# Kernel tuning notes

Hardware: AMD Instinct MI355X
Metric: run time of the kernel (lower is better)

## Reference

```python
import jax, jax.numpy as jnp
import numpy as np

NUM_HEADS = 16
HEAD_DIM = 64
WINDOW = 512
D_MODEL = NUM_HEADS * HEAD_DIM
BATCH = 2
SEQ = 2048


def setup_inputs() -> dict:
    key = jax.random.key(0)
    k1, k2, k3 = jax.random.split(key, 3)
    x = jax.random.normal(k1, (BATCH, SEQ, D_MODEL), dtype=jnp.float32)
    # Dense layer params (lecun_normal-like scale for stability)
    qkv_kernel = jax.random.normal(k2, (D_MODEL, 3 * NUM_HEADS * HEAD_DIM), dtype=jnp.float32) / np.sqrt(D_MODEL)
    qkv_bias = jnp.zeros((3 * NUM_HEADS * HEAD_DIM,), dtype=jnp.float32)
    out_kernel = jax.random.normal(k3, (NUM_HEADS * HEAD_DIM, D_MODEL), dtype=jnp.float32) / np.sqrt(D_MODEL)
    out_bias = jnp.zeros((D_MODEL,), dtype=jnp.float32)
    return {"x": x, "qkv_kernel": qkv_kernel, "qkv_bias": qkv_bias,
            "out_kernel": out_kernel, "out_bias": out_bias}


def reference(x, qkv_kernel, qkv_bias, out_kernel, out_bias):
    b, s, d = x.shape
    qkv = x @ qkv_kernel + qkv_bias                       # (b, s, 3*H*hd)
    qkv = qkv.reshape(b, s, 3, NUM_HEADS, HEAD_DIM)
    q = qkv[:, :, 0].transpose(0, 2, 1, 3)                # (b, H, s, hd)
    k = qkv[:, :, 1].transpose(0, 2, 1, 3)
    v = qkv[:, :, 2].transpose(0, 2, 1, 3)
    scale = 1.0 / jnp.sqrt(jnp.float32(HEAD_DIM)).astype(x.dtype)
    scores = jnp.einsum('bhqd,bhkd->bhqk', q, k) * scale  # (b, H, s, s)
    rows = jnp.arange(s)[:, None]
    cols = jnp.arange(s)[None, :]
    window_mask = (rows - cols >= 0) & (rows - cols < WINDOW)
    scores = jnp.where(window_mask[None, None], scores, jnp.asarray(-1e9, scores.dtype))
    attn = jax.nn.softmax(scores, axis=-1)
    out = jnp.einsum('bhqk,bhkd->bhqd', attn, v)          # (b, H, s, hd)
    out = out.transpose(0, 2, 1, 3).reshape(b, s, -1)
    return out @ out_kernel + out_bias
```

## Files before the change

### kernel.cpp

```cpp
#include <hip/hip_runtime.h>
#include <cstdint>
#include <cstddef>

#define NUM_HEADS 16
#define HEAD_DIM  64
#define WINDOW    512
#define D_MODEL   1024
#define BATCH     2
#define SEQ       2048
#define MTOT      (BATCH*SEQ)
#define NQKV      (3*D_MODEL)

typedef short bf16x8 __attribute__((ext_vector_type(8)));
typedef float f32x4  __attribute__((ext_vector_type(4)));

__device__ __forceinline__ f32x4 mfma16(bf16x8 a, bf16x8 b, f32x4 c) {
  return __builtin_amdgcn_mfma_f32_16x16x32_bf16(a, b, c, 0, 0, 0);
}

__device__ __forceinline__ unsigned short f2bf(float f) {
  unsigned int u = __float_as_uint(f);
  u += 0x7fffu + ((u >> 16) & 1u);
  return (unsigned short)(u >> 16);
}
__device__ __forceinline__ float bf2f(unsigned short b) {
  return __uint_as_float(((unsigned int)b) << 16);
}

__device__ __forceinline__ void gld16(const unsigned short* g, unsigned short* l) {
  __builtin_amdgcn_global_load_lds(
      (const __attribute__((address_space(1))) unsigned int*)g,
      (__attribute__((address_space(3))) unsigned int*)l, 16, 0, 0);
}

__global__ __launch_bounds__(256) void prep_kernel(const float* __restrict__ x,
                                                   const float* __restrict__ qkv_w,
                                                   const float* __restrict__ out_w,
                                                   unsigned short* __restrict__ Xb,
                                                   unsigned short* __restrict__ Wq,
                                                   unsigned short* __restrict__ Wo) {
  __shared__ float tile[32][33];
  const int bid = blockIdx.x, t = threadIdx.x;
  if (bid < 4096) {
    int i = (bid * 256 + t) * 4;
    float4 v = *(const float4*)(x + i);
    ushort4 o;
    o.x = f2bf(v.x); o.y = f2bf(v.y); o.z = f2bf(v.z); o.w = f2bf(v.w);
    *(ushort4*)(Xb + i) = o;
    return;
  }
  const float* in; unsigned short* out; int R, C, bx, by;
  if (bid < 7168) { int b2 = bid - 4096; in = qkv_w; out = Wq; R = D_MODEL; C = NQKV; bx = b2 % 96; by = b2 / 96; }
  else            { int b2 = bid - 7168; in = out_w; out = Wo; R = D_MODEL; C = D_MODEL; bx = b2 & 31; by = b2 >> 5; }
  int tx = t & 31, ty = t >> 5;
  int c0 = bx * 32, r0 = by * 32;
#pragma unroll
  for (int i = 0; i < 32; i += 8)
    tile[ty + i][tx] = in[(size_t)(r0 + ty + i) * C + c0 + tx];
  __syncthreads();
#pragma unroll
  for (int i = 0; i < 32; i += 8)
    out[(size_t)(c0 + ty + i) * R + r0 + tx] = f2bf(tile[tx][ty + i]);
}

template<bool SWAP, int K>
__device__ __forceinline__ void gemm_mainloop512(const unsigned short* __restrict__ A,
                                                 const unsigned short* __restrict__ Bt,
                                                 int m0, int n0,
                                                 unsigned short* sA, unsigned short* sB,
                                                 f32x4 (&acc)[2][4]) {
  const int t = threadIdx.x;
  const int lane = t & 63, wave = t >> 6;
  const int wr = wave >> 1, wc = wave & 1;
  const int lhi = lane >> 4, llo = lane & 15;
  f32x4 zero = {0.f, 0.f, 0.f, 0.f};
#pragma unroll
  for (int i = 0; i < 2; ++i)
#pragma unroll
    for (int j = 0; j < 4; ++j) acc[i][j] = zero;

  const int cswz = (((t & 3) ^ ((t >> 3) & 3)) << 3);
  const unsigned short* gA = A  + (size_t)(m0 + (t >> 2)) * K + cswz;
  const unsigned short* gB = Bt + (size_t)(n0 + (t >> 2)) * K + cswz;
  const int ldsT = t * 8;
  const int rsw  = (lhi ^ ((llo >> 1) & 3)) * 8;
  const int aoff = (wr * 32 + llo) * 32 + rsw;
  const int boff = (wc * 64 + llo) * 32 + rsw;
  constexpr int nIter = K / 32;

  auto stage = [&](int s) {
    unsigned short* dA = sA + (s % 3) * 4096;
    unsigned short* dB = sB + (s % 3) * 4096;
    gld16(gA + s * 32, dA + ldsT);
    gld16(gB + s * 32, dB + ldsT);
  };

  stage(0);
  stage(1);
#pragma unroll
  for (int it = 0; it < nIter; ++it) {
    if (it + 1 < nIter) asm volatile("s_waitcnt vmcnt(2)\n\ts_barrier" ::: "memory");
    else                asm volatile("s_waitcnt vmcnt(0)\n\ts_barrier" ::: "memory");
    if (it + 2 < nIter) stage(it + 2);
    const unsigned short* cA = sA + (it % 3) * 4096;
    const unsigned short* cB = sB + (it % 3) * 4096;
    bf16x8 af[2], bfr[4];
#pragma unroll
    for (int i = 0; i < 2; ++i) af[i]  = *(const bf16x8*)(cA + aoff + i * 512);
#pragma unroll
    for (int j = 0; j < 4; ++j)  bfr[j] = *(const bf16x8*)(cB + boff + j * 512);
#pragma unroll
    for (int i = 0; i < 2; ++i)
#pragma unroll
      for (int j = 0; j < 4; ++j)
        acc[i][j] = SWAP ? mfma16(bfr[j], af[i], acc[i][j])
                         : mfma16(af[i], bfr[j], acc[i][j]);
  }
}

template<bool SWAP>
__device__ __forceinline__ void gemm_mainloop_256q(const unsigned short* __restrict__ A,
                                                   const unsigned short* __restrict__ Bt,
                                                   int m0, int n0,
                                                   unsigned short* sA, unsigned short* sB,
                                                   f32x4 (&acc)[8][4]) {
  constexpr int K = D_MODEL;
  constexpr int nT = K / 64;
  const int t = threadIdx.x, lane = t & 63, wave = t >> 6;
  const int wr = wave >> 2, wc = wave & 3;
  const int lhi = lane >> 4, llo = lane & 15;
  f32x4 zero = {0.f, 0.f, 0.f, 0.f};
#pragma unroll
  for (int i = 0; i < 8; ++i)
#pragma unroll
    for (int j = 0; j < 4; ++j) acc[i][j] = zero;

  const int r6 = t >> 3;
  const int chunkS = (t & 7) ^ (r6 & 7);
  const unsigned short* gAr = A  + (size_t)(m0 + r6) * K + chunkS * 8;
  const unsigned short* gBr = Bt + (size_t)(n0 + (r6 >> 5) * 64 + (r6 & 31)) * K + chunkS * 8;
  const int dstT = t * 8;

  const int k0off = (lhi ^ (llo & 7)) * 8;
  const int k1off = k0off ^ 32;
  const int aRow = (wr * 64 + llo) * 64;
  const int bRow = (wc * 32 + llo) * 64;

  auto stA = [&](int j, int mh) {
    unsigned short* d = sA + (((j & 1) << 1) + mh) * 8192 + dstT;
    const unsigned short* g = gAr + (size_t)(mh * 64) * K + j * 64;
    gld16(g, d);
    gld16(g + (size_t)128 * K, d + 4096);
  };
  auto stB = [&](int j, int nh) {
    unsigned short* d = sB + (((j & 1) << 1) + nh) * 8192 + dstT;
    const unsigned short* g = gBr + (size_t)(nh * 32) * K + j * 64;
    gld16(g, d);
    gld16(g + (size_t)128 * K, d + 4096);
  };

#define QPHASE(JV, MH, NH, STG)                                                  \
  {                                                                              \
    const unsigned short* cA = sA + ((((JV) & 1) << 1) + (MH)) * 8192;           \
    const unsigned short* cB = sB + ((((JV) & 1) << 1) + (NH)) * 8192;           \
    bf16x8 af[4][2], bfv[2][2];                                                  \
    _Pragma("unroll") for (int i2 = 0; i2 < 4; ++i2) {                           \
      af[i2][0] = *(const bf16x8*)(cA + aRow + i2 * 1024 + k0off);               \
      af[i2][1] = *(const bf16x8*)(cA + aRow + i2 * 1024 + k1off);               \
    }                                                                            \
    _Pragma("unroll") for (int j2 = 0; j2 < 2; ++j2) {                           \
      bfv[j2][0] = *(const bf16x8*)(cB + bRow + j2 * 1024 + k0off);              \
      bfv[j2][1] = *(const bf16x8*)(cB + bRow + j2 * 1024 + k1off);              \
    }                                                                            \
    STG;                                                                         \
    asm volatile("s_barrier" ::: "memory");                                      \
    __builtin_amdgcn_s_setprio(1);                                               \
    _Pragma("unroll") for (int i2 = 0; i2 < 4; ++i2)                             \
      _Pragma("unroll") for (int j2 = 0; j2 < 2; ++j2) {                         \
        f32x4& ac = acc[(MH) * 4 + i2][(NH) * 2 + j2];                           \
        ac = SWAP ? mfma16(bfv[j2][0], af[i2][0], ac)                            \
                  : mfma16(af[i2][0], bfv[j2][0], ac);                           \
        ac = SWAP ? mfma16(bfv[j2][1], af[i2][1], ac)                            \
                  : mfma16(af[i2][1], bfv[j2][1], ac);                           \
      }                                                                          \
    __builtin_amdgcn_s_setprio(0);                                               \
  }

  stA(0, 0); stB(0, 0); stB(0, 1); stA(0, 1); stA(1, 0);

  for (int j = 0; j < nT - 1; ++j) {
    asm volatile("s_waitcnt vmcnt(6)\n\ts_barrier" ::: "memory");
    QPHASE(j, 0, 0, { stB(j + 1, 0); });
    asm volatile("s_waitcnt vmcnt(6)\n\ts_barrier" ::: "memory");
    QPHASE(j, 0, 1, { stB(j + 1, 1); });
    asm volatile("s_waitcnt vmcnt(6)\n\ts_barrier" ::: "memory");
    QPHASE(j, 1, 0, { stA(j + 1, 1); });
    asm volatile("s_waitcnt vmcnt(6)\n\ts_barrier" ::: "memory");
    QPHASE(j, 1, 1, { if (j + 2 < nT) stA(j + 2, 0); });
  }
  asm volatile("s_waitcnt vmcnt(4)\n\ts_barrier" ::: "memory");
  QPHASE(nT - 1, 0, 0, {});
  asm volatile("s_waitcnt vmcnt(2)\n\ts_barrier" ::: "memory");
  QPHASE(nT - 1, 0, 1, {});
  asm volatile("s_waitcnt vmcnt(0)\n\ts_barrier" ::: "memory");
  QPHASE(nT - 1, 1, 0, {});
  asm volatile("s_barrier" ::: "memory");
  QPHASE(nT - 1, 1, 1, {});
#undef QPHASE
}

__global__ __launch_bounds__(512, 2) void qkv_gemm_kernel(const unsigned short* __restrict__ Xb,
                                                          const unsigned short* __restrict__ Wt,
                                                          const float* __restrict__ bias,
                                                          unsigned short* __restrict__ Qw,
                                                          unsigned short* __restrict__ Kw,
                                                          unsigned short* __restrict__ Vtw) {
  __shared__ __align__(16) unsigned short sA[2 * 2 * 8192];
  __shared__ __align__(16) unsigned short sB[2 * 2 * 8192];
  f32x4 acc[8][4];
  const int m0 = blockIdx.y * 256, n0 = blockIdx.x * 256;
  const int t = threadIdx.x, lane = t & 63, wave = t >> 6;
  const int wr = wave >> 2, wc = wave & 3, lhi = lane >> 4, llo = lane & 15;

  if (n0 < 2048) {
    gemm_mainloop_256q<false>(Xb, Wt, m0, n0, sA, sB, acc);
    const int c = n0 >> 10;
    unsigned short* __restrict__ Dst = (c == 0) ? Qw : Kw;
    const float qs = (c == 0) ? 0.125f : 1.0f;
#pragma unroll
    for (int mi = 0; mi < 8; ++mi) {
#pragma unroll
      for (int nj = 0; nj < 4; ++nj) {
        int n = n0 + wc * 64 + nj * 16 + llo;
        float bv = bias[n];
        int h = (n >> 6) & 15, d = n & 63;
#pragma unroll
        for (int r = 0; r < 4; ++r) {
          int m = m0 + wr * 128 + mi * 16 + lhi * 4 + r;
          int b = m >> 11, s = m & 2047;
          int bh = b * 16 + h;
          Dst[((size_t)(bh * 2048 + s)) * 64 + d] = f2bf((acc[mi][nj][r] + bv) * qs);
        }
      }
    }
  } else {
    gemm_mainloop_256q<true>(Xb, Wt, m0, n0, sA, sB, acc);
#pragma unroll
    for (int mi = 0; mi < 8; ++mi) {
      int m = m0 + wr * 128 + mi * 16 + llo;
      int b = m >> 11, s = m & 2047;
#pragma unroll
      for (int nj = 0; nj < 4; ++nj) {
        int nb = n0 + wc * 64 + nj * 16 + lhi * 4;
        float4 bv = *(const float4*)(bias + nb);
        int h = (nb >> 6) & 15, dbase = nb & 63;
        int bh = b * 16 + h;
        float bvr[4] = {bv.x, bv.y, bv.z, bv.w};
#pragma unroll
        for (int r = 0; r < 4; ++r)
          Vtw[(size_t)(bh * 64 + dbase + r) * 2048 + s] = f2bf(acc[mi][nj][r] + bvr[r]);
      }
    }
  }
}

__global__ __launch_bounds__(512) void attn_kernel(const unsigned short* __restrict__ Qw,
                                                   const unsigned short* __restrict__ Kw,
                                                   const unsigned short* __restrict__ Vtw,
                                                   unsigned short* __restrict__ AO) {
  __shared__ __align__(16) unsigned short sK[3][64 * 64];
  __shared__ __align__(16) unsigned short sV[3][64 * 64];
  __shared__ __align__(16) unsigned short sP[8][16 * 72];
  const int t = threadIdx.x, lane = t & 63, wave = t >> 6;
  const int lhi = lane >> 4, llo = lane & 15;
  const int bh = blockIdx.x;
  const int q0 = (15 - blockIdx.y) << 7;
  const unsigned short* Qb = Qw  + (size_t)bh * 2048 * 64;
  const unsigned short* Kb = Kw  + (size_t)bh * 2048 * 64;
  const unsigned short* Vb = Vtw + (size_t)bh * 64 * 2048;

  const int qw = q0 + wave * 16;
  const int qrow = qw + llo;
  bf16x8 qf0 = *(const bf16x8*)(Qb + (size_t)qrow * 64 + lhi * 8);
  bf16x8 qf1 = *(const bf16x8*)(Qb + (size_t)qrow * 64 + 32 + lhi * 8);

  const int srow = t >> 3;
  const int scol = ((t & 7) ^ (srow & 7)) * 8;
  const int cpos  = (lhi ^ (llo & 7)) * 8;
  const int cposx = cpos ^ 32;

  float m_i = -1e30f, l_i = 0.f;
  f32x4 o[4];
  f32x4 zero = {0.f, 0.f, 0.f, 0.f};
#pragma unroll
  for (int td = 0; td < 4; ++td) o[td] = zero;

  const int kt_lo = (q0 > 511) ? ((q0 - 511) >> 6) : 0;
  const int kt_hi = (q0 + 127) >> 6;

  auto stageKV = [&](int j) {
    const int k0 = j << 6;
    unsigned short* dK = sK[j % 3];
    unsigned short* dV = sV[j % 3];
    gld16(Kb + (size_t)(k0 + srow) * 64 + scol, dK + t * 8);
    gld16(Vb + (size_t)srow * 2048 + k0 + scol, dV + t * 8);
  };

  stageKV(kt_lo);
  stageKV(kt_lo + 1);

  for (int kt = kt_lo; kt <= kt_hi; ++kt) {
    if (kt < kt_hi) asm volatile("s_waitcnt vmcnt(2)\n\ts_barrier" ::: "memory");
    else            asm volatile("s_waitcnt vmcnt(0)\n\ts_barrier" ::: "memory");
    if (kt + 2 <= kt_hi) stageKV(kt + 2);
    const int k0 = kt << 6;
    if (k0 > qw + 15 || k0 + 63 < qw - (WINDOW - 1)) continue;

    const unsigned short* bK = sK[kt % 3];
    const unsigned short* bV = sV[kt % 3];

    f32x4 st[4];
#pragma unroll
    for (int tk = 0; tk < 4; ++tk) {
      const unsigned short* kr = bK + (tk * 16 + llo) * 64;
      bf16x8 kf0 = *(const bf16x8*)(kr + cpos);
      bf16x8 kf1 = *(const bf16x8*)(kr + cposx);
      f32x4 z = zero;
      z = mfma16(kf0, qf0, z);
      z = mfma16(kf1, qf1, z);
      st[tk] = z;
    }

    const bool interior = (k0 >= qw - (WINDOW - 1 - 15)) && (k0 + 63 <= qw);
    const int kb = k0 + lhi * 4;
    float mx = -1e30f;
    if (interior) {
#pragma unroll
      for (int tk = 0; tk < 4; ++tk)
#pragma unroll
        for (int r = 0; r < 4; ++r) mx = fmaxf(mx, st[tk][r]);
    } else {
#pragma unroll
      for (int tk = 0; tk < 4; ++tk)
#pragma unroll
        for (int r = 0; r < 4; ++r) {
          int key = kb + tk * 16 + r;
          bool ok = (key <= qrow) && (qrow - key < WINDOW);
          float s = ok ? st[tk][r] : -1e30f;
          st[tk][r] = s;
          mx = fmaxf(mx, s);
        }
    }
    mx = fmaxf(mx, __shfl_xor(mx, 16));
    mx = fmaxf(mx, __shfl_xor(mx, 32));
    float mn = fmaxf(m_i, mx);
    float a  = __expf(m_i - mn);
    float rs = 0.f;
    unsigned short* pw = &sP[wave][llo * 72];
#pragma unroll
    for (int tk = 0; tk < 4; ++tk) {
      ushort4 pb;
      pb.x = f2bf(__expf(st[tk][0] - mn));
      pb.y = f2bf(__expf(st[tk][1] - mn));
      pb.z = f2bf(__expf(st[tk][2] - mn));
      pb.w = f2bf(__expf(st[tk][3] - mn));
      *(ushort4*)(pw + tk * 16 + lhi * 4) = pb;
      rs += bf2f(pb.x) + bf2f(pb.y) + bf2f(pb.z) + bf2f(pb.w);
    }
    rs += __shfl_xor(rs, 16);
    rs += __shfl_xor(rs, 32);
    l_i = l_i * a + rs;
    m_i = mn;

    float aR[4];
#pragma unroll
    for (int r = 0; r < 4; ++r) aR[r] = __shfl(a, lhi * 4 + r);
#pragma unroll
    for (int td = 0; td < 4; ++td)
#pragma unroll
      for (int r = 0; r < 4; ++r) o[td][r] *= aR[r];

    bf16x8 pf0 = *(const bf16x8*)(pw + lhi * 8);
    bf16x8 pf1 = *(const bf16x8*)(pw + 32 + lhi * 8);
#pragma unroll
    for (int td = 0; td < 4; ++td) {
      const unsigned short* vr = bV + (td * 16 + llo) * 64;
      bf16x8 vf0 = *(const bf16x8*)(vr + cpos);
      bf16x8 vf1 = *(const bf16x8*)(vr + cposx);
      o[td] = mfma16(pf0, vf0, o[td]);
      o[td] = mfma16(pf1, vf1, o[td]);
    }
  }

  float lR[4];
#pragma unroll
  for (int r = 0; r < 4; ++r) lR[r] = 1.f / __shfl(l_i, lhi * 4 + r);
  const int b = bh >> 4, h = bh & 15;
#pragma unroll
  for (int td = 0; td < 4; ++td)
#pragma unroll
    for (int r = 0; r < 4; ++r) {
      int qr = q0 + wave * 16 + lhi * 4 + r;
      AO[(size_t)(b * 2048 + qr) * 1024 + h * 64 + td * 16 + llo] = f2bf(o[td][r] * lR[r]);
    }
}

__global__ __launch_bounds__(512, 2) void out_gemm_kernel(const unsigned short* __restrict__ AO,
                                                          const unsigned short* __restrict__ Wt,
                                                          const float* __restrict__ bias,
                                                          float* __restrict__ out) {
  __shared__ __align__(16) unsigned short sA[3][128 * 32];
  __shared__ __align__(16) unsigned short sB[3][128 * 32];
  f32x4 acc[2][4];
  const int m0 = blockIdx.y * 128, n0 = blockIdx.x * 128;
  gemm_mainloop512<false, D_MODEL>(AO, Wt, m0, n0, sA[0], sB[0], acc);

  const int t = threadIdx.x, lane = t & 63, wave = t >> 6;
  const int wr = wave >> 1, wc = wave & 1, lhi = lane >> 4, llo = lane & 15;
#pragma unroll
  for (int ti = 0; ti < 2; ++ti)
#pragma unroll
    for (int tj = 0; tj < 4; ++tj) {
      int n = n0 + wc * 64 + tj * 16 + llo;
      float bv = bias[n];
#pragma unroll
      for (int r = 0; r < 4; ++r) {
        int m = m0 + wr * 32 + ti * 16 + lhi * 4 + r;
        out[(size_t)m * D_MODEL + n] = acc[ti][tj][r] + bv;
      }
    }
}

extern "C" void kernel_launch(void* const* d_in, const int* in_sizes, int n_in,
                              void* d_out, int out_size, void* d_ws, size_t ws_size,
                              hipStream_t stream) {
  const float* x      = (const float*)d_in[0];
  const float* qkv_w  = (const float*)d_in[1];
  const float* qkv_b  = (const float*)d_in[2];
  const float* out_w  = (const float*)d_in[3];
  const float* out_b  = (const float*)d_in[4];
  float* out = (float*)d_out;
  char* ws = (char*)d_ws;

  unsigned short* Xb  = (unsigned short*)(ws);
  unsigned short* Wq  = (unsigned short*)(ws + ((size_t)8  << 20));
  unsigned short* Wo  = (unsigned short*)(ws + ((size_t)14 << 20));
  unsigned short* Qw  = (unsigned short*)(ws + ((size_t)16 << 20));
  unsigned short* Kw  = (unsigned short*)(ws + ((size_t)24 << 20));
  unsigned short* Vtw = (unsigned short*)(ws + ((size_t)32 << 20));
  unsigned short* AO  = (unsigned short*)(ws + ((size_t)40 << 20));

  prep_kernel<<<8192, 256, 0, stream>>>(x, qkv_w, out_w, Xb, Wq, Wo);
  qkv_gemm_kernel<<<dim3(NQKV / 256, MTOT / 256), 512, 0, stream>>>(Xb, Wq, qkv_b, Qw, Kw, Vtw);
  attn_kernel<<<dim3(BATCH * NUM_HEADS, SEQ / 128), 512, 0, stream>>>(Qw, Kw, Vtw, AO);
  out_gemm_kernel<<<dim3(D_MODEL / 128, MTOT / 128), 512, 0, stream>>>(AO, Wo, out_b, out);
}
```

Baseline: 169.0 us.

## Reorder GEMM mainloop quadrants to reuse A/B fragments in registers across phases

Restructures the 256x256 GEMM mainloop from four independent LDS-read+MFMA phases into a snake order (00, 01, 11, 10) that keeps the A and B fragments in registers. This cuts LDS reads per k-step from 4 A and 4 B fragment loads to 2 of each. It also changes the prefetch schedule, waitcnt thresholds and barrier placement, and adds sched_barriers. In exchange it needs more live registers (two B fragment sets) and more barriers per iteration, and the new buffer-reuse timing must stay race-free.

```diff
diff --git a/kernel.cpp b/kernel.cpp
--- a/kernel.cpp
+++ b/kernel.cpp
@@ -147,66 +147,105 @@
   const int bRow = (wc * 32 + llo) * 64;
 
   auto stA = [&](int j, int mh) {
-    unsigned short* d = sA + (((j & 1) << 1) + mh) * 8192 + dstT;
+    unsigned short* d = sA + ((j & 1) * 2 + mh) * 8192 + dstT;
     const unsigned short* g = gAr + (size_t)(mh * 64) * K + j * 64;
     gld16(g, d);
     gld16(g + (size_t)128 * K, d + 4096);
   };
   auto stB = [&](int j, int nh) {
-    unsigned short* d = sB + (((j & 1) << 1) + nh) * 8192 + dstT;
+    unsigned short* d = sB + ((j & 1) * 2 + nh) * 8192 + dstT;
     const unsigned short* g = gBr + (size_t)(nh * 32) * K + j * 64;
     gld16(g, d);
     gld16(g + (size_t)128 * K, d + 4096);
   };
-
-#define QPHASE(JV, MH, NH, STG)                                                  \
-  {                                                                              \
-    const unsigned short* cA = sA + ((((JV) & 1) << 1) + (MH)) * 8192;           \
-    const unsigned short* cB = sB + ((((JV) & 1) << 1) + (NH)) * 8192;           \
-    bf16x8 af[4][2], bfv[2][2];                                                  \
-    _Pragma("unroll") for (int i2 = 0; i2 < 4; ++i2) {                           \
-      af[i2][0] = *(const bf16x8*)(cA + aRow + i2 * 1024 + k0off);               \
-      af[i2][1] = *(const bf16x8*)(cA + aRow + i2 * 1024 + k1off);               \
-    }                                                                            \
-    _Pragma("unroll") for (int j2 = 0; j2 < 2; ++j2) {                           \
-      bfv[j2][0] = *(const bf16x8*)(cB + bRow + j2 * 1024 + k0off);              \
-      bfv[j2][1] = *(const bf16x8*)(cB + bRow + j2 * 1024 + k1off);              \
-    }                                                                            \
-    STG;                                                                         \
-    asm volatile("s_barrier" ::: "memory");                                      \
-    __builtin_amdgcn_s_setprio(1);                                               \
-    _Pragma("unroll") for (int i2 = 0; i2 < 4; ++i2)                             \
-      _Pragma("unroll") for (int j2 = 0; j2 < 2; ++j2) {                         \
-        f32x4& ac = acc[(MH) * 4 + i2][(NH) * 2 + j2];                           \
-        ac = SWAP ? mfma16(bfv[j2][0], af[i2][0], ac)                            \
-                  : mfma16(af[i2][0], bfv[j2][0], ac);                           \
-        ac = SWAP ? mfma16(bfv[j2][1], af[i2][1], ac)                            \
-                  : mfma16(af[i2][1], bfv[j2][1], ac);                           \
-      }                                                                          \
-    __builtin_amdgcn_s_setprio(0);                                               \
-  }
-
-  stA(0, 0); stB(0, 0); stB(0, 1); stA(0, 1); stA(1, 0);
-
+  auto rdA = [&](bf16x8 (&af)[4][2], int j, int mh) {
+    const unsigned short* cA = sA + ((j & 1) * 2 + mh) * 8192;
+#pragma unroll
+    for (int mi = 0; mi < 4; ++mi) {
+      af[mi][0] = *(const bf16x8*)(cA + aRow + mi * 1024 + k0off);
+      af[mi][1] = *(const bf16x8*)(cA + aRow + mi * 1024 + k1off);
+    }
+  };
+  auto rdB = [&](bf16x8 (&bf)[2][2], int j, int nh) {
+    const unsigned short* cB = sB + ((j & 1) * 2 + nh) * 8192;
+#pragma unroll
+    for (int nj = 0; nj < 2; ++nj) {
+      bf[nj][0] = *(const bf16x8*)(cB + bRow + nj * 1024 + k0off);
+      bf[nj][1] = *(const bf16x8*)(cB + bRow + nj * 1024 + k1off);
+    }
+  };
+
+#define MFMA_QUAD(MH, NH, AF, BF)                                        \
+  __builtin_amdgcn_s_setprio(1);                                         \
+  _Pragma("unroll") for (int mi = 0; mi < 4; ++mi)                       \
+    _Pragma("unroll") for (int nj = 0; nj < 2; ++nj) {                   \
+      f32x4& ac = acc[(MH) * 4 + mi][(NH) * 2 + nj];                     \
+      ac = SWAP ? mfma16(BF[nj][0], AF[mi][0], ac)                       \
+                : mfma16(AF[mi][0], BF[nj][0], ac);                      \
+      ac = SWAP ? mfma16(BF[nj][1], AF[mi][1], ac)                       \
+                : mfma16(AF[mi][1], BF[nj][1], ac);                      \
+    }                                                                    \
+  __builtin_amdgcn_s_setprio(0);
+
+  stA(0, 0); stB(0, 0); stB(0, 1); stA(0, 1);
+  asm volatile("s_waitcnt vmcnt(4)" ::: "memory");
+  __builtin_amdgcn_s_barrier();
+
+  bf16x8 a[4][2], b0[2][2], b1[2][2];
   for (int j = 0; j < nT - 1; ++j) {
-    asm volatile("s_waitcnt vmcnt(6)\n\ts_barrier" ::: "memory");
-    QPHASE(j, 0, 0, { stB(j + 1, 0); });
-    asm volatile("s_waitcnt vmcnt(6)\n\ts_barrier" ::: "memory");
-    QPHASE(j, 0, 1, { stB(j + 1, 1); });
-    asm volatile("s_waitcnt vmcnt(6)\n\ts_barrier" ::: "memory");
-    QPHASE(j, 1, 0, { stA(j + 1, 1); });
-    asm volatile("s_waitcnt vmcnt(6)\n\ts_barrier" ::: "memory");
-    QPHASE(j, 1, 1, { if (j + 2 < nT) stA(j + 2, 0); });
-  }
-  asm volatile("s_waitcnt vmcnt(4)\n\ts_barrier" ::: "memory");
-  QPHASE(nT - 1, 0, 0, {});
-  asm volatile("s_waitcnt vmcnt(2)\n\ts_barrier" ::: "memory");
-  QPHASE(nT - 1, 0, 1, {});
-  asm volatile("s_waitcnt vmcnt(0)\n\ts_barrier" ::: "memory");
-  QPHASE(nT - 1, 1, 0, {});
-  asm volatile("s_barrier" ::: "memory");
-  QPHASE(nT - 1, 1, 1, {});
-#undef QPHASE
+    rdA(a, j, 0); rdB(b0, j, 0);
+    stA(j + 1, 0);
+    asm volatile("s_waitcnt vmcnt(4) lgkmcnt(8)" ::: "memory");
+    __builtin_amdgcn_s_barrier();
+    asm volatile("s_waitcnt lgkmcnt(0)" ::: "memory");
+    __builtin_amdgcn_sched_barrier(0);
+    MFMA_QUAD(0, 0, a, b0);
+    __builtin_amdgcn_s_barrier();
+    rdB(b1, j, 1);
+    stB(j + 1, 0);
+    asm volatile("s_waitcnt vmcnt(4)" ::: "memory");
+    __builtin_amdgcn_s_barrier();
+    asm volatile("s_waitcnt lgkmcnt(0)" ::: "memory");
+    __builtin_amdgcn_sched_barrier(0);
+    MFMA_QUAD(0, 1, a, b1);
+    __builtin_amdgcn_s_barrier();
+    rdA(a, j, 1);
+    stB(j + 1, 1);
+    __builtin_amdgcn_s_barrier();
+    asm volatile("s_waitcnt lgkmcnt(0)" ::: "memory");
+    __builtin_amdgcn_sched_barrier(0);
+    MFMA_QUAD(1, 1, a, b1);
+    __builtin_amdgcn_s_barrier();
+    stA(j + 1, 1);
+    asm volatile("s_waitcnt vmcnt(4)" ::: "memory");
+    __builtin_amdgcn_s_barrier();
+    __builtin_amdgcn_sched_barrier(0);
+    MFMA_QUAD(1, 0, a, b0);
+    __builtin_amdgcn_s_barrier();
+  }
+  {
+    const int j = nT - 1;
+    rdA(a, j, 0); rdB(b0, j, 0);
+    asm volatile("s_waitcnt vmcnt(2) lgkmcnt(8)" ::: "memory");
+    __builtin_amdgcn_s_barrier();
+    asm volatile("s_waitcnt lgkmcnt(0)" ::: "memory");
+    __builtin_amdgcn_sched_barrier(0);
+    MFMA_QUAD(0, 0, a, b0);
+    __builtin_amdgcn_s_barrier();
+    rdB(b1, j, 1);
+    asm volatile("s_waitcnt vmcnt(0)" ::: "memory");
+    __builtin_amdgcn_s_barrier();
+    asm volatile("s_waitcnt lgkmcnt(0)" ::: "memory");
+    __builtin_amdgcn_sched_barrier(0);
+    MFMA_QUAD(0, 1, a, b1);
+    __builtin_amdgcn_s_barrier();
+    rdA(a, j, 1);
+    asm volatile("s_waitcnt lgkmcnt(0)" ::: "memory");
+    __builtin_amdgcn_sched_barrier(0);
+    MFMA_QUAD(1, 1, a, b1);
+    MFMA_QUAD(1, 0, a, b0);
+  }
+#undef MFMA_QUAD
 }
 
 __global__ __launch_bounds__(512, 2) void qkv_gemm_kernel(const unsigned short* __restrict__ Xb,
```

After: 166.2 us. Within noise of the previous version (-1.7%).
